# Optimization experiments

Measured on AMD Instinct MI355X. Metric: run time of the kernel, lower is better.

Reference implementation:

```python
import jax, jax.numpy as jnp
import numpy as np

N, E, IN, HID, OUT, H = 10000, 320000, 256, 128, 128, 4
SLOPE = 0.2

def setup_inputs() -> dict:
    key = jax.random.key(0)
    ks = jax.random.split(key, 12)
    s = lambda d: 1.0 / np.sqrt(d)
    return {
        "x": jax.random.normal(ks[0], (N, IN), jnp.float32),
        "edge_index": jax.random.randint(ks[1], (2, E), 0, N, jnp.int32),
        "W1": jax.random.normal(ks[2], (IN, H * HID), jnp.float32) * s(IN),
        "a_src1": jax.random.normal(ks[3], (H, HID), jnp.float32) * s(HID),
        "a_dst1": jax.random.normal(ks[4], (H, HID), jnp.float32) * s(HID),
        "b1": jnp.zeros((H * HID,), jnp.float32),
        "W2": jax.random.normal(ks[5], (H * HID, H * OUT), jnp.float32) * s(H * HID),
        "a_src2": jax.random.normal(ks[6], (H, OUT), jnp.float32) * s(OUT),
        "a_dst2": jax.random.normal(ks[7], (H, OUT), jnp.float32) * s(OUT),
        "b2": jnp.zeros((OUT,), jnp.float32),
    }

def _gat_layer(x, src, dst, W, a_src, a_dst, bias, concat, C):
    n = x.shape[0]
    h = (x @ W).reshape(n, H, C)                      # [N,H,C]
    alpha_s = jnp.einsum('nhc,hc->nh', h, a_src)      # [N,H]
    alpha_d = jnp.einsum('nhc,hc->nh', h, a_dst)
    e = jax.nn.leaky_relu(alpha_s[src] + alpha_d[dst], SLOPE)  # [E,H]
    # segment softmax over incoming edges of each dst node
    m = jax.ops.segment_max(e, dst, num_segments=n)   # [N,H]
    m = jnp.where(jnp.isfinite(m), m, 0.0)
    ex = jnp.exp(e - m[dst])
    denom = jax.ops.segment_sum(ex, dst, num_segments=n)
    alpha = ex / (denom[dst] + 1e-16)                 # [E,H]
    msg = h[src] * alpha[:, :, None]                  # [E,H,C]
    out = jax.ops.segment_sum(msg, dst, num_segments=n)  # [N,H,C]
    out = out.reshape(n, H * C) if concat else out.mean(axis=1)
    return out + bias

def reference(x, edge_index, W1, a_src1, a_dst1, b1, W2, a_src2, a_dst2, b2):
    n = x.shape[0]
    loops = jnp.arange(n, dtype=edge_index.dtype)
    src = jnp.concatenate([edge_index[0], loops])
    dst = jnp.concatenate([edge_index[1], loops])
    h = _gat_layer(x, src, dst, W1, a_src1, a_dst1, b1, True, HID)
    h = jax.nn.relu(h)  # dropout is identity in eval mode
    out = _gat_layer(h, src, dst, W2, a_src2, a_dst2, b2, False, OUT)
    return out
```

## Files before the change

kernel.cpp:

```cpp
#include <hip/hip_runtime.h>
#include <hip/hip_fp16.h>
#include <math.h>

#define Nn 10000
#define Ee 320000
#define EE 330000
#define INF_ 256
#define NH 4
#define OUTC 128
#define F1 512
#define F2 512
#define SLOPE 0.2f
#define STRIDE 80
#define LDK 40
#define MT 157

#define SC_BLOCKS 1290
#define TW1_BLOCKS 512
#define TW2_BLOCKS 1024
#define GEMM_GRID 640

static __device__ __forceinline__ float lrelu(float x) { return fmaxf(x, SLOPE * x); }

using frag_ab = __attribute__((ext_vector_type(8))) _Float16;
using frag_c  = __attribute__((ext_vector_type(4))) float;

__global__ void prep(const int* __restrict__ ei, int* counts, int* __restrict__ csr,
                     const float* __restrict__ W1, const float* __restrict__ W2,
                     _Float16* __restrict__ w1t, _Float16* __restrict__ w2t) {
    int b = blockIdx.x, t = threadIdx.x;
    if (b < SC_BLOCKS) {
        int e = b * 256 + t;
        if (e < EE) {
            int src, dst;
            if (e < Ee) { src = ei[e]; dst = ei[Ee + e]; }
            else        { src = e - Ee; dst = e - Ee; }
            int slot = atomicAdd(&counts[dst], 1);
            if (slot < STRIDE) csr[dst * STRIDE + slot] = src;
        }
    } else if (b < SC_BLOCKS + TW1_BLOCKS) {
        int bb = b - SC_BLOCKS;
        int n = (bb & 7) * 64 + (t & 63);
        int k = (bb >> 3) * 4 + (t >> 6);
        w1t[(size_t)n * INF_ + k] = (_Float16)W1[(size_t)k * F1 + n];
    } else {
        int bb = b - SC_BLOCKS - TW1_BLOCKS;
        int n = (bb & 7) * 64 + (t & 63);
        int k = (bb >> 3) * 4 + (t >> 6);
        w2t[(size_t)n * F1 + k] = (_Float16)W2[(size_t)k * F2 + n];
    }
}

template <bool AF32>
static __device__ void gemm_tile(const _Float16* __restrict__ Ah,
                                 const float* __restrict__ Af,
                                 const _Float16* __restrict__ BT,
                                 _Float16* __restrict__ C,
                                 const float* __restrict__ a_src,
                                 const float* __restrict__ a_dst,
                                 float* __restrict__ as_out,
                                 float* __restrict__ ad_out,
                                 int K, int bmi, int head,
                                 _Float16* As, _Float16* Bs) {
    const int tid = threadIdx.x;
    const int wave = tid >> 6, lane = tid & 63;
    const int q = lane >> 4, ml = lane & 15;
    const int bm = bmi * 64, bn = head * 128;
    const int srow = tid >> 2, scol = (tid & 3) * 8;

    frag_c acc[8];
#pragma unroll
    for (int f = 0; f < 8; f++)
#pragma unroll
        for (int r = 0; r < 4; r++) acc[f][r] = 0.f;

    for (int k0 = 0; k0 < K; k0 += 32) {
        int gm = bm + srow;
        frag_ab av;
        if (gm < Nn) {
            if constexpr (AF32) {
                const float* Ap = Af + (size_t)gm * K + k0 + scol;
                float4 v0 = *(const float4*)Ap;
                float4 v1 = *(const float4*)(Ap + 4);
                av[0] = (_Float16)v0.x; av[1] = (_Float16)v0.y;
                av[2] = (_Float16)v0.z; av[3] = (_Float16)v0.w;
                av[4] = (_Float16)v1.x; av[5] = (_Float16)v1.y;
                av[6] = (_Float16)v1.z; av[7] = (_Float16)v1.w;
            } else {
                av = *(const frag_ab*)(Ah + (size_t)gm * K + k0 + scol);
            }
        } else {
#pragma unroll
            for (int j = 0; j < 8; j++) av[j] = (_Float16)0.f;
        }
        *(frag_ab*)&As[srow * LDK + scol] = av;
        *(frag_ab*)&Bs[srow * LDK + scol] =
            *(const frag_ab*)(BT + (size_t)(bn + srow) * K + k0 + scol);
        *(frag_ab*)&Bs[(64 + srow) * LDK + scol] =
            *(const frag_ab*)(BT + (size_t)(bn + 64 + srow) * K + k0 + scol);
        __syncthreads();
        frag_ab a = *(frag_ab*)&As[(wave * 16 + ml) * LDK + q * 8];
#pragma unroll
        for (int f = 0; f < 8; f++) {
            frag_ab b = *(frag_ab*)&Bs[(f * 16 + ml) * LDK + q * 8];
            acc[f] = __builtin_amdgcn_mfma_f32_16x16x32_f16(a, b, acc[f], 0, 0, 0);
        }
        __syncthreads();
    }
    float asum[4] = {}, dsum[4] = {};
#pragma unroll
    for (int f = 0; f < 8; f++) {
        int cl = f * 16 + ml;
        int col = bn + cl;
        float sa = a_src[head * 128 + cl];
        float da = a_dst[head * 128 + cl];
#pragma unroll
        for (int r = 0; r < 4; r++) {
            int row = bm + wave * 16 + q * 4 + r;
            if (row < Nn) C[(size_t)row * (NH * 128) + col] = (_Float16)acc[f][r];
            asum[r] += acc[f][r] * sa;
            dsum[r] += acc[f][r] * da;
        }
    }
#pragma unroll
    for (int r = 0; r < 4; r++) {
#pragma unroll
        for (int off = 1; off < 16; off <<= 1) {
            asum[r] += __shfl_xor(asum[r], off);
            dsum[r] += __shfl_xor(dsum[r], off);
        }
    }
    if (ml == 0) {
#pragma unroll
        for (int r = 0; r < 4; r++) {
            int row = bm + wave * 16 + q * 4 + r;
            if (row < Nn) {
                as_out[(size_t)head * Nn + row] = asum[r];
                ad_out[(size_t)head * Nn + row] = dsum[r];
            }
        }
    }
}

__global__ __launch_bounds__(256) void gemm1(const float* __restrict__ x,
                                             const _Float16* __restrict__ w1t,
                                             _Float16* __restrict__ hh,
                                             const float* __restrict__ a_src,
                                             const float* __restrict__ a_dst,
                                             float* __restrict__ as_out,
                                             float* __restrict__ ad_out) {
    __shared__ _Float16 As[64 * LDK];
    __shared__ _Float16 Bs[128 * LDK];
    int bid = blockIdx.x;
    int m8 = bid & 7, rest = bid >> 3;
    int h = rest & 3, mhi = rest >> 2;
    int m = mhi * 8 + m8;
    if (m >= MT) return;
    gemm_tile<true>(nullptr, x, w1t, hh, a_src, a_dst, as_out, ad_out, INF_, m, h, As, Bs);
}

__global__ __launch_bounds__(256) void gemm2(const _Float16* __restrict__ aggh,
                                             const _Float16* __restrict__ w2t,
                                             _Float16* __restrict__ hh,
                                             const float* __restrict__ a_src,
                                             const float* __restrict__ a_dst,
                                             float* __restrict__ as_out,
                                             float* __restrict__ ad_out) {
    __shared__ _Float16 As[64 * LDK];
    __shared__ _Float16 Bs[128 * LDK];
    int bid = blockIdx.x;
    int m8 = bid & 7, rest = bid >> 3;
    int h = rest & 3, mhi = rest >> 2;
    int m = mhi * 8 + m8;
    if (m >= MT) return;
    gemm_tile<false>(aggh, nullptr, w2t, hh, a_src, a_dst, as_out, ad_out, F1, m, h, As, Bs);
}

__global__ __launch_bounds__(256) void passAB1(const int* __restrict__ counts,
                                               const int* __restrict__ csr,
                                               const float* __restrict__ as,
                                               const float* __restrict__ ad,
                                               const _Float16* __restrict__ hh,
                                               const float* __restrict__ b1,
                                               _Float16* __restrict__ agg) {
    __shared__ int2 ew[16][84];
    int head = blockIdx.x & 3;
    int qw = threadIdx.x >> 4;
    int l = threadIdx.x & 15;
    int n = (blockIdx.x >> 2) * 16 + qw;
    int deg = counts[n]; if (deg > STRIDE) deg = STRIDE;
    int pdeg = (deg + 7) & ~7;
    const float* ash = as + (size_t)head * Nn;
    float adh = ad[(size_t)head * Nn + n];
    int base = n * STRIDE;
    float m = -1e30f;
    for (int k = l; k < pdeg; k += 16) {
        int src = 0; float v = -1e30f;
        if (k < deg) {
            src = csr[base + k];
            v = lrelu(ash[src] + adh);
        }
        ew[qw][k] = make_int2(src, __float_as_int(v));
        m = fmaxf(m, v);
    }
    m = fmaxf(m, __shfl_xor(m, 1));
    m = fmaxf(m, __shfl_xor(m, 2));
    m = fmaxf(m, __shfl_xor(m, 4));
    m = fmaxf(m, __shfl_xor(m, 8));
    float s = 0.f;
    for (int k = l; k < pdeg; k += 16) {
        float e = __expf(__int_as_float(ew[qw][k].y) - m);
        ew[qw][k].y = __float_as_int(e);
        s += e;
    }
    s += __shfl_xor(s, 1);
    s += __shfl_xor(s, 2);
    s += __shfl_xor(s, 4);
    s += __shfl_xor(s, 8);
    float inv = 1.f / (s + 1e-16f);
    int c = head * 128 + (l << 3);
    float acc[8] = {};
    for (int kk = 0; kk < pdeg; kk += 8) {
        int2 pj[8];
#pragma unroll
        for (int j = 0; j < 8; j++) pj[j] = ew[qw][kk + j];
#pragma unroll
        for (int j = 0; j < 8; j++) {
            float w = __int_as_float(pj[j].y);
            frag_ab r = *(const frag_ab*)(hh + (size_t)pj[j].x * F1 + c);
#pragma unroll
            for (int u = 0; u < 8; u++) acc[u] = fmaf((float)r[u], w, acc[u]);
        }
    }
    _Float16 oh[8];
#pragma unroll
    for (int j = 0; j < 8; j++)
        oh[j] = (_Float16)fmaxf(acc[j] * inv + b1[c + j], 0.f);
    *(float4*)&agg[(size_t)n * F1 + c] = *(float4*)oh;
}

__global__ __launch_bounds__(256) void passC(const int* __restrict__ counts,
                                             const int* __restrict__ csr,
                                             const float* __restrict__ as,
                                             const float* __restrict__ ad,
                                             const _Float16* __restrict__ hh,
                                             const float* __restrict__ b2,
                                             float* __restrict__ out) {
    __shared__ int   esrc[4][80];
    __shared__ float ewgt[4][4][80];
    int w = threadIdx.x >> 6;
    int lane = threadIdx.x & 63;
    int h = lane >> 4, i = lane & 15;
    int n = blockIdx.x * 4 + w;
    int deg = counts[n]; if (deg > STRIDE) deg = STRIDE;
    int pdeg = (deg + 7) & ~7;
    float adh = ad[(size_t)h * Nn + n];
    const float* ash = as + (size_t)h * Nn;
    int base = n * STRIDE;
    float m = -1e30f;
    for (int k = i; k < pdeg; k += 16) {
        int src = 0; float v = -1e30f;
        if (k < deg) {
            src = csr[base + k];
            v = lrelu(ash[src] + adh);
        }
        if (h == 0) esrc[w][k] = src;
        ewgt[w][h][k] = v;
        m = fmaxf(m, v);
    }
    m = fmaxf(m, __shfl_xor(m, 1));
    m = fmaxf(m, __shfl_xor(m, 2));
    m = fmaxf(m, __shfl_xor(m, 4));
    m = fmaxf(m, __shfl_xor(m, 8));
    float s = 0.f;
    for (int k = i; k < pdeg; k += 16) {
        float e = __expf(ewgt[w][h][k] - m);
        ewgt[w][h][k] = e;
        s += e;
    }
    s += __shfl_xor(s, 1);
    s += __shfl_xor(s, 2);
    s += __shfl_xor(s, 4);
    s += __shfl_xor(s, 8);
    float scale = 0.25f / (s + 1e-16f);
    int c = lane << 3;
    float acc[8] = {};
    for (int kk = 0; kk < pdeg; kk += 8) {
        int s8[8]; float w8[8];
#pragma unroll
        for (int j = 0; j < 8; j++) { s8[j] = esrc[w][kk + j]; w8[j] = ewgt[w][h][kk + j]; }
#pragma unroll
        for (int j = 0; j < 8; j++) {
            frag_ab r = *(const frag_ab*)(hh + (size_t)s8[j] * F2 + c);
#pragma unroll
            for (int u = 0; u < 8; u++) acc[u] = fmaf((float)r[u], w8[j], acc[u]);
        }
    }
#pragma unroll
    for (int u = 0; u < 8; u++) {
        acc[u] *= scale;
        acc[u] += __shfl_xor(acc[u], 16);
        acc[u] += __shfl_xor(acc[u], 32);
    }
    if (h == 0) {
        float o[8];
#pragma unroll
        for (int j = 0; j < 8; j++) o[j] = acc[j] + b2[(i << 3) + j];
        *(float4*)&out[(size_t)n * OUTC + (i << 3)]     = *(float4*)&o[0];
        *(float4*)&out[(size_t)n * OUTC + (i << 3) + 4] = *(float4*)&o[4];
    }
}

extern "C" void kernel_launch(void* const* d_in, const int* in_sizes, int n_in,
                              void* d_out, int out_size, void* d_ws, size_t ws_size,
                              hipStream_t stream) {
    const float* x      = (const float*)d_in[0];
    const int*   ei     = (const int*)d_in[1];
    const float* W1     = (const float*)d_in[2];
    const float* a_src1 = (const float*)d_in[3];
    const float* a_dst1 = (const float*)d_in[4];
    const float* b1     = (const float*)d_in[5];
    const float* W2     = (const float*)d_in[6];
    const float* a_src2 = (const float*)d_in[7];
    const float* a_dst2 = (const float*)d_in[8];
    const float* b2     = (const float*)d_in[9];
    float* out = (float*)d_out;

    char* w = (char*)d_ws;
    _Float16* hh   = (_Float16*)w; w += (size_t)Nn * F1 * 2;
    _Float16* aggh = (_Float16*)w; w += (size_t)Nn * F1 * 2;
    _Float16* w1t  = (_Float16*)w; w += (size_t)F1 * INF_ * 2;
    _Float16* w2t  = (_Float16*)w; w += (size_t)F2 * F1 * 2;
    float* as1     = (float*)w;    w += (size_t)NH * Nn * 4;
    float* ad1     = (float*)w;    w += (size_t)NH * Nn * 4;
    float* as2     = (float*)w;    w += (size_t)NH * Nn * 4;
    float* ad2     = (float*)w;    w += (size_t)NH * Nn * 4;
    int* csr       = (int*)w;      w += (size_t)Nn * STRIDE * 4;
    int* counts    = (int*)w;      w += (size_t)Nn * 4;

    (void)hipMemsetAsync(counts, 0, Nn * sizeof(int), stream);
    prep<<<SC_BLOCKS + TW1_BLOCKS + TW2_BLOCKS, 256, 0, stream>>>(
        ei, counts, csr, W1, W2, w1t, w2t);

    gemm1<<<GEMM_GRID, 256, 0, stream>>>(x, w1t, hh, a_src1, a_dst1, as1, ad1);
    passAB1<<<(Nn / 16) * NH, 256, 0, stream>>>(counts, csr, as1, ad1, hh, b1, aggh);

    gemm2<<<GEMM_GRID, 256, 0, stream>>>(aggh, w2t, hh, a_src2, a_dst2, as2, ad2);
    passC<<<Nn / 4, 256, 0, stream>>>(counts, csr, as2, ad2, hh, b2, out);
}
```

Baseline: 199.7 us.

## Overlap edge scatter with GEMM1, split layer-2 aggregation per head with atomics

Moves CSR edge bucketing out of the prep kernel and into extra blocks of the first GEMM launch, so the atomic scatter runs alongside the tensor-core tiles. The counts memset becomes part of prep, which is now ordered before the scatter. The final aggregation now uses one block per head per 16 nodes, like layer 1, and combines the four heads into the output with float atomicAdd, which requires a memset of the output. This raises parallelism in the last pass at the cost of atomic traffic and makes the float summation order nondeterministic. GEMM grids are also remapped to drop idle blocks.

Result: slower. 299.1 us (+49.8%).

```diff
diff --git a/kernel.cpp b/kernel.cpp
--- a/kernel.cpp
+++ b/kernel.cpp
@@ -15,39 +15,35 @@
 #define LDK 40
 #define MT 157
 
-#define SC_BLOCKS 1290
 #define TW1_BLOCKS 512
 #define TW2_BLOCKS 1024
-#define GEMM_GRID 640
+#define ZC_BLOCKS 40
+#define PREP_GRID (TW1_BLOCKS + TW2_BLOCKS + ZC_BLOCKS)
+#define GEMM_TILES (MT * NH)
+#define SCAT_BLOCKS 430
+#define G1_GRID (GEMM_TILES + SCAT_BLOCKS)
 
 static __device__ __forceinline__ float lrelu(float x) { return fmaxf(x, SLOPE * x); }
 
 using frag_ab = __attribute__((ext_vector_type(8))) _Float16;
 using frag_c  = __attribute__((ext_vector_type(4))) float;
 
-__global__ void prep(const int* __restrict__ ei, int* counts, int* __restrict__ csr,
-                     const float* __restrict__ W1, const float* __restrict__ W2,
+__global__ void prep(int* counts, const float* __restrict__ W1,
+                     const float* __restrict__ W2,
                      _Float16* __restrict__ w1t, _Float16* __restrict__ w2t) {
     int b = blockIdx.x, t = threadIdx.x;
-    if (b < SC_BLOCKS) {
-        int e = b * 256 + t;
-        if (e < EE) {
-            int src, dst;
-            if (e < Ee) { src = ei[e]; dst = ei[Ee + e]; }
-            else        { src = e - Ee; dst = e - Ee; }
-            int slot = atomicAdd(&counts[dst], 1);
-            if (slot < STRIDE) csr[dst * STRIDE + slot] = src;
-        }
-    } else if (b < SC_BLOCKS + TW1_BLOCKS) {
-        int bb = b - SC_BLOCKS;
-        int n = (bb & 7) * 64 + (t & 63);
-        int k = (bb >> 3) * 4 + (t >> 6);
+    if (b < TW1_BLOCKS) {
+        int n = (b & 7) * 64 + (t & 63);
+        int k = (b >> 3) * 4 + (t >> 6);
         w1t[(size_t)n * INF_ + k] = (_Float16)W1[(size_t)k * F1 + n];
-    } else {
-        int bb = b - SC_BLOCKS - TW1_BLOCKS;
+    } else if (b < TW1_BLOCKS + TW2_BLOCKS) {
+        int bb = b - TW1_BLOCKS;
         int n = (bb & 7) * 64 + (t & 63);
         int k = (bb >> 3) * 4 + (t >> 6);
         w2t[(size_t)n * F1 + k] = (_Float16)W2[(size_t)k * F2 + n];
+    } else {
+        int i = (b - TW1_BLOCKS - TW2_BLOCKS) * 256 + t;
+        if (i < Nn) counts[i] = 0;
     }
 }
 
@@ -142,21 +138,32 @@
     }
 }
 
-__global__ __launch_bounds__(256) void gemm1(const float* __restrict__ x,
-                                             const _Float16* __restrict__ w1t,
-                                             _Float16* __restrict__ hh,
-                                             const float* __restrict__ a_src,
-                                             const float* __restrict__ a_dst,
-                                             float* __restrict__ as_out,
-                                             float* __restrict__ ad_out) {
+__global__ __launch_bounds__(256) void gemm1_scatter(const float* __restrict__ x,
+                                                     const _Float16* __restrict__ w1t,
+                                                     _Float16* __restrict__ hh,
+                                                     const float* __restrict__ a_src,
+                                                     const float* __restrict__ a_dst,
+                                                     float* __restrict__ as_out,
+                                                     float* __restrict__ ad_out,
+                                                     const int* __restrict__ ei,
+                                                     int* counts, int* __restrict__ csr) {
     __shared__ _Float16 As[64 * LDK];
     __shared__ _Float16 Bs[128 * LDK];
     int bid = blockIdx.x;
-    int m8 = bid & 7, rest = bid >> 3;
-    int h = rest & 3, mhi = rest >> 2;
-    int m = mhi * 8 + m8;
-    if (m >= MT) return;
-    gemm_tile<true>(nullptr, x, w1t, hh, a_src, a_dst, as_out, ad_out, INF_, m, h, As, Bs);
+    if (bid < GEMM_TILES) {
+        int m = bid % MT, h = bid / MT;
+        gemm_tile<true>(nullptr, x, w1t, hh, a_src, a_dst, as_out, ad_out,
+                        INF_, m, h, As, Bs);
+    } else {
+        int bi = bid - GEMM_TILES;
+        for (int e = bi * 256 + threadIdx.x; e < EE; e += SCAT_BLOCKS * 256) {
+            int src, dst;
+            if (e < Ee) { src = ei[e]; dst = ei[Ee + e]; }
+            else        { src = e - Ee; dst = e - Ee; }
+            int slot = atomicAdd(&counts[dst], 1);
+            if (slot < STRIDE) csr[dst * STRIDE + slot] = src;
+        }
+    }
 }
 
 __global__ __launch_bounds__(256) void gemm2(const _Float16* __restrict__ aggh,
@@ -168,12 +175,8 @@
                                              float* __restrict__ ad_out) {
     __shared__ _Float16 As[64 * LDK];
     __shared__ _Float16 Bs[128 * LDK];
-    int bid = blockIdx.x;
-    int m8 = bid & 7, rest = bid >> 3;
-    int h = rest & 3, mhi = rest >> 2;
-    int m = mhi * 8 + m8;
-    if (m >= MT) return;
-    gemm_tile<false>(aggh, nullptr, w2t, hh, a_src, a_dst, as_out, ad_out, F1, m, h, As, Bs);
+    gemm_tile<false>(aggh, nullptr, w2t, hh, a_src, a_dst, as_out, ad_out,
+                     F1, blockIdx.x, blockIdx.y, As, Bs);
 }
 
 __global__ __launch_bounds__(256) void passAB1(const int* __restrict__ counts,
@@ -239,33 +242,31 @@
     *(float4*)&agg[(size_t)n * F1 + c] = *(float4*)oh;
 }
 
-__global__ __launch_bounds__(256) void passC(const int* __restrict__ counts,
-                                             const int* __restrict__ csr,
-                                             const float* __restrict__ as,
-                                             const float* __restrict__ ad,
-                                             const _Float16* __restrict__ hh,
-                                             const float* __restrict__ b2,
-                                             float* __restrict__ out) {
-    __shared__ int   esrc[4][80];
-    __shared__ float ewgt[4][4][80];
-    int w = threadIdx.x >> 6;
-    int lane = threadIdx.x & 63;
-    int h = lane >> 4, i = lane & 15;
-    int n = blockIdx.x * 4 + w;
+__global__ __launch_bounds__(256) void passAB2a(const int* __restrict__ counts,
+                                                const int* __restrict__ csr,
+                                                const float* __restrict__ as,
+                                                const float* __restrict__ ad,
+                                                const _Float16* __restrict__ hh,
+                                                const float* __restrict__ b2,
+                                                float* __restrict__ out) {
+    __shared__ int2 ew[16][84];
+    int head = blockIdx.x & 3;
+    int qw = threadIdx.x >> 4;
+    int l = threadIdx.x & 15;
+    int n = (blockIdx.x >> 2) * 16 + qw;
     int deg = counts[n]; if (deg > STRIDE) deg = STRIDE;
     int pdeg = (deg + 7) & ~7;
-    float adh = ad[(size_t)h * Nn + n];
-    const float* ash = as + (size_t)h * Nn;
+    const float* ash = as + (size_t)head * Nn;
+    float adh = ad[(size_t)head * Nn + n];
     int base = n * STRIDE;
     float m = -1e30f;
-    for (int k = i; k < pdeg; k += 16) {
+    for (int k = l; k < pdeg; k += 16) {
         int src = 0; float v = -1e30f;
         if (k < deg) {
             src = csr[base + k];
             v = lrelu(ash[src] + adh);
         }
-        if (h == 0) esrc[w][k] = src;
-        ewgt[w][h][k] = v;
+        ew[qw][k] = make_int2(src, __float_as_int(v));
         m = fmaxf(m, v);
     }
     m = fmaxf(m, __shfl_xor(m, 1));
@@ -273,41 +274,39 @@
     m = fmaxf(m, __shfl_xor(m, 4));
     m = fmaxf(m, __shfl_xor(m, 8));
     float s = 0.f;
-    for (int k = i; k < pdeg; k += 16) {
-        float e = __expf(ewgt[w][h][k] - m);
-        ewgt[w][h][k] = e;
+    for (int k = l; k < pdeg; k += 16) {
+        float e = __expf(__int_as_float(ew[qw][k].y) - m);
+        ew[qw][k].y = __float_as_int(e);
         s += e;
     }
     s += __shfl_xor(s, 1);
     s += __shfl_xor(s, 2);
     s += __shfl_xor(s, 4);
     s += __shfl_xor(s, 8);
-    float scale = 0.25f / (s + 1e-16f);
-    int c = lane << 3;
+    float inv = 1.f / (s + 1e-16f);
+    int c = head * 128 + (l << 3);
     float acc[8] = {};
     for (int kk = 0; kk < pdeg; kk += 8) {
-        int s8[8]; float w8[8];
-#pragma unroll
-        for (int j = 0; j < 8; j++) { s8[j] = esrc[w][kk + j]; w8[j] = ewgt[w][h][kk + j]; }
+        int2 pj[8];
+#pragma unroll
+        for (int j = 0; j < 8; j++) pj[j] = ew[qw][kk + j];
 #pragma unroll
         for (int j = 0; j < 8; j++) {
-            frag_ab r = *(const frag_ab*)(hh + (size_t)s8[j] * F2 + c);
-#pragma unroll
-            for (int u = 0; u < 8; u++) acc[u] = fmaf((float)r[u], w8[j], acc[u]);
-        }
-    }
-#pragma unroll
-    for (int u = 0; u < 8; u++) {
-        acc[u] *= scale;
-        acc[u] += __shfl_xor(acc[u], 16);
-        acc[u] += __shfl_xor(acc[u], 32);
-    }
-    if (h == 0) {
-        float o[8];
-#pragma unroll
-        for (int j = 0; j < 8; j++) o[j] = acc[j] + b2[(i << 3) + j];
-        *(float4*)&out[(size_t)n * OUTC + (i << 3)]     = *(float4*)&o[0];
-        *(float4*)&out[(size_t)n * OUTC + (i << 3) + 4] = *(float4*)&o[4];
+            float w = __int_as_float(pj[j].y);
+            frag_ab r = *(const frag_ab*)(hh + (size_t)pj[j].x * F2 + c);
+#pragma unroll
+            for (int u = 0; u < 8; u++) acc[u] = fmaf((float)r[u], w, acc[u]);
+        }
+    }
+    float qq = 0.25f * inv;
+    int oc = l << 3;
+    float* op = out + (size_t)n * OUTC + oc;
+    if (head == 0) {
+#pragma unroll
+        for (int j = 0; j < 8; j++) atomicAdd(op + j, fmaf(acc[j], qq, b2[oc + j]));
+    } else {
+#pragma unroll
+        for (int j = 0; j < 8; j++) atomicAdd(op + j, acc[j] * qq);
     }
 }
 
@@ -338,13 +337,14 @@
     int* csr       = (int*)w;      w += (size_t)Nn * STRIDE * 4;
     int* counts    = (int*)w;      w += (size_t)Nn * 4;
 
-    (void)hipMemsetAsync(counts, 0, Nn * sizeof(int), stream);
-    prep<<<SC_BLOCKS + TW1_BLOCKS + TW2_BLOCKS, 256, 0, stream>>>(
-        ei, counts, csr, W1, W2, w1t, w2t);
-
-    gemm1<<<GEMM_GRID, 256, 0, stream>>>(x, w1t, hh, a_src1, a_dst1, as1, ad1);
+    (void)hipMemsetAsync(out, 0, (size_t)Nn * OUTC * sizeof(float), stream);
+
+    prep<<<PREP_GRID, 256, 0, stream>>>(counts, W1, W2, w1t, w2t);
+
+    gemm1_scatter<<<G1_GRID, 256, 0, stream>>>(x, w1t, hh, a_src1, a_dst1, as1, ad1,
+                                               ei, counts, csr);
     passAB1<<<(Nn / 16) * NH, 256, 0, stream>>>(counts, csr, as1, ad1, hh, b1, aggh);
 
-    gemm2<<<GEMM_GRID, 256, 0, stream>>>(aggh, w2t, hh, a_src2, a_dst2, as2, ad2);
-    passC<<<Nn / 4, 256, 0, stream>>>(counts, csr, as2, ad2, hh, b2, out);
-}
+    gemm2<<<dim3(MT, NH), 256, 0, stream>>>(aggh, w2t, hh, a_src2, a_dst2, as2, ad2);
+    passAB2a<<<(Nn / 16) * NH, 256, 0, stream>>>(counts, csr, as2, ad2, hh, b2, out);
+}
```
